# Kernel tuning notes

Hardware: AMD Instinct MI355X
Metric: run time of the kernel (lower is better)

The kernel has to match this reference:

```python
import jax, jax.numpy as jnp
import numpy as np

N = 16384      # nodes
E = 262144     # edges (avg degree 16)
R = 9          # relation types
D_IN = 384     # embed_size
D_H = 768      # hidden_size
N_CLASSES = 5


def setup_inputs() -> dict:
    key = jax.random.key(0)
    ks = jax.random.split(key, 11)
    s = 0.02
    return {
        "x": jax.random.normal(ks[0], (N, D_IN), jnp.float32),
        "edge_index": jax.random.randint(ks[1], (2, E), 0, N, dtype=jnp.int64)
        if jax.config.jax_enable_x64 else jax.random.randint(ks[1], (2, E), 0, N).astype(jnp.int32),
        "edge_type": jax.random.randint(ks[2], (E,), 0, R).astype(jnp.int32),
        "rel_W": jax.random.normal(ks[3], (R, D_H, D_IN), jnp.float32) * s,
        "rel_b": jax.random.normal(ks[4], (R, D_H), jnp.float32) * s,
        "norm_constants": jnp.ones((R,), jnp.float32),
        "mp_lin_W": jax.random.normal(ks[5], (D_H, D_H), jnp.float32) * s,
        "mp_lin_b": jax.random.normal(ks[6], (D_H,), jnp.float32) * s,
        "mp_self_W": jax.random.normal(ks[7], (D_H, D_H), jnp.float32) * s,
        "mp_self_b": jax.random.normal(ks[8], (D_H,), jnp.float32) * s,
        "out_W": jax.random.normal(ks[9], (N_CLASSES, D_H), jnp.float32) * s,
        "out_b": jax.random.normal(ks[10], (N_CLASSES,), jnp.float32) * s,
    }


def reference(x, edge_index, edge_type, rel_W, rel_b, norm_constants,
              mp_lin_W, mp_lin_b, mp_self_W, mp_self_b, out_W, out_b):
    n = x.shape[0]
    src = edge_index[0]  # j : message source (x_j)
    dst = edge_index[1]  # i : aggregation target

    # --- RelationAwareMP ---
    # edge_weights[i, j] from x @ x.T, computed per edge (identical math)
    ew = jnp.einsum('ed,ed->e', x[dst], x[src])                  # [E]
    norm = ew / norm_constants[edge_type]                        # [E]
    # per-relation linear applied to all nodes, then gathered per edge
    h = jnp.einsum('nd,rhd->rnh', x, rel_W) + rel_b[:, None, :]  # [R,N,H]
    msg = h[edge_type, src]                                      # [E,H]
    aggr = jax.ops.segment_sum(norm[:, None] * msg, dst, num_segments=n)
    x1 = jax.nn.relu(aggr)                                       # [N,H]

    # --- MP (add aggregation + self transform) ---
    self_x = x1 @ mp_self_W.T + mp_self_b
    hm = x1 @ mp_lin_W.T + mp_lin_b
    aggr2 = jax.ops.segment_sum(hm[src], dst, num_segments=n)
    x2 = jax.nn.relu(aggr2 + self_x)                             # [N,H]

    # --- readout ---
    pooled = x2.mean(axis=0)                                     # [H]
    return pooled @ out_W.T + out_b                              # [N_CLASSES]
```

## Files before the change

### kernel.cpp

```cpp
#include <hip/hip_runtime.h>

typedef unsigned char  u8;
typedef unsigned short u16;
typedef unsigned int   u32;

#define NN   16384
#define EE   262144
#define RR   9
#define DIN  384
#define DH   768
#define KSU  3456
#define KS   3488
#define NPB  4
#define PCOP 16

typedef float  f32x4 __attribute__((ext_vector_type(4)));
typedef float  f32x2 __attribute__((ext_vector_type(2)));
typedef u32    u32x2 __attribute__((ext_vector_type(2)));
typedef __bf16 b16x8 __attribute__((ext_vector_type(8)));

__device__ __forceinline__ u16 f2bf(float f){
  u32 u = __builtin_bit_cast(u32, f);
  u += 0x7fffu + ((u >> 16) & 1u);
  return (u16)(u >> 16);
}
__device__ __forceinline__ float bf2f(u16 h){
  u32 u = ((u32)h) << 16;
  return __builtin_bit_cast(float, u);
}
__device__ __forceinline__ u32 pkbf(float a, float b){
  return (u32)f2bf(a) | ((u32)f2bf(b) << 16);
}
__device__ __forceinline__ void gll16(const void* g, void* l){
  __builtin_amdgcn_global_load_lds((const __attribute__((address_space(1))) void*)g,
                                   (__attribute__((address_space(3))) void*)l, 16, 0, 0);
}
template<int N> __device__ __forceinline__ float dppror(float v){
  return __builtin_bit_cast(float,
    __builtin_amdgcn_update_dpp(0, __builtin_bit_cast(int, v), 0x120+N, 0xF, 0xF, true));
}
__device__ __forceinline__ float swz16(float v){
  return __builtin_bit_cast(float,
    __builtin_amdgcn_ds_swizzle(__builtin_bit_cast(int, v), 0x401F));
}

__global__ void k_count(const int* __restrict__ dst, int* __restrict__ counts){
  const int e = blockIdx.x*256 + threadIdx.x;
  if (e < EE) atomicAdd(&counts[dst[e]], 1);
}

__global__ __launch_bounds__(1024) void k_scan(const int* __restrict__ counts,
                                               int* __restrict__ starts,
                                               int* __restrict__ cursor){
  __shared__ int tot[1024];
  const int t = threadIdx.x;
  int loc[16]; int s = 0;
  #pragma unroll
  for (int j=0;j<16;j++){ loc[j] = counts[t*16+j]; s += loc[j]; }
  tot[t] = s;
  __syncthreads();
  for (int o=1;o<1024;o<<=1){
    int v = (t>=o) ? tot[t-o] : 0;
    __syncthreads();
    tot[t] += v;
    __syncthreads();
  }
  int run = tot[t] - s;
  #pragma unroll
  for (int j=0;j<16;j++){ starts[t*16+j] = run; cursor[t*16+j] = run; run += loc[j]; }
  if (t == 1023) starts[NN] = run;
}

__global__ void k_place(const int* __restrict__ src, const int* __restrict__ dst,
                        const int* __restrict__ et, int* __restrict__ cursor,
                        int* __restrict__ sp){
  const int e = blockIdx.x*256 + threadIdx.x;
  if (e < EE){
    const int p = atomicAdd(&cursor[dst[e]], 1);
    sp[p] = (int)(((u32)et[e] << 28) | (u32)src[e]);
  }
}

__global__ void k_convW1(const float* __restrict__ rW, const float* __restrict__ rb,
                         u16* __restrict__ Wst){
  const int hh = blockIdx.y;
  const int k  = blockIdx.x*256 + threadIdx.x;
  if (k >= KS) return;
  float v;
  if (k < KSU){ const int r = k / DIN; const int d = k - r*DIN;
                v = rW[((long)r*DH + hh)*DIN + d]; }
  else if (k < KSU + RR){ const int r = k - KSU; v = rb[(long)r*DH + hh]; }
  else v = 0.f;
  Wst[(long)hh*KS + k] = f2bf(v);
}

__global__ void k_convW2(const float* __restrict__ lW, const float* __restrict__ sW,
                         u16* __restrict__ WB){
  const int idx = blockIdx.x*256 + threadIdx.x;
  const float v = (idx < DH*DH) ? lW[idx] : sW[idx - DH*DH];
  WB[idx] = f2bf(v);
}

__global__ __launch_bounds__(256, 3) void k_phase1f(const float* __restrict__ x,
                                                    const int* __restrict__ sp,
                                                    const float* __restrict__ nc,
                                                    const int* __restrict__ starts,
                                                    u16* __restrict__ s){
  const int wv = threadIdx.x >> 6;
  const int l  = threadIdx.x & 63;
  const int i  = blockIdx.x*4 + wv;
  const float* xdp = x + (long)i*DIN;
  const f32x4 xq = *(const f32x4*)(xdp + 4*l);
  const f32x2 xr = *(const f32x2*)(xdp + 256 + 2*l);
  float acc[RR][6];
  float cacc[RR];
  #pragma unroll
  for (int r=0;r<RR;r++){
    cacc[r] = 0.f;
    #pragma unroll
    for (int j=0;j<6;j++) acc[r][j] = 0.f;
  }
  const int e0 = starts[i], e1 = starts[i+1];
  f32x4 Aq={0,0,0,0}, Bq={0,0,0,0}, Cq={0,0,0,0}, Dq={0,0,0,0};
  f32x2 Ar={0,0}, Br={0,0}, Cr={0,0}, Dr={0,0};
  u32 qA=0,qB=0,qC=0,qD=0;
  #define LDE(S, QQ, IDX) { const int pe_=(IDX); if (pe_ < e1){ QQ = (u32)sp[pe_]; \
      const float* xs_ = x + (long)(QQ & 0x3FFFu)*DIN; \
      S##q = *(const f32x4*)(xs_ + 4*l); \
      S##r = *(const f32x2*)(xs_ + 256 + 2*l); } }
  LDE(A,qA,e0) LDE(B,qB,e0+1) LDE(C,qC,e0+2) LDE(D,qD,e0+3)
  #define DOT(uq,ur) (xq.x*uq.x + xq.y*uq.y + xq.z*uq.z + xq.w*uq.w \
                    + xr.x*ur.x + xr.y*ur.y)
  #define UPD(R,P,cq,cr) { cacc[R] += P; \
      acc[R][0] += P*cq.x; acc[R][1] += P*cq.y; acc[R][2] += P*cq.z; \
      acc[R][3] += P*cq.w; acc[R][4] += P*cr.x; acc[R][5] += P*cr.y; }
  #define SW(RQ,P,cq,cr) switch (RQ){ \
      case 0: UPD(0,P,cq,cr); break; case 1: UPD(1,P,cq,cr); break; \
      case 2: UPD(2,P,cq,cr); break; case 3: UPD(3,P,cq,cr); break; \
      case 4: UPD(4,P,cq,cr); break; case 5: UPD(5,P,cq,cr); break; \
      case 6: UPD(6,P,cq,cr); break; case 7: UPD(7,P,cq,cr); break; \
      default: UPD(8,P,cq,cr); break; }
  for (int p=e0; p<e1; p+=4){
    const f32x4 aq=Aq, bq=Bq, cq=Cq, dq=Dq;
    const f32x2 ar=Ar, br=Br, cr=Cr, dr=Dr;
    const u32 qa=qA, qb=qB, qc=qC, qd=qD;
    const bool h1 = p+1<e1, h2 = p+2<e1, h3 = p+3<e1;
    LDE(A,qA,p+4) LDE(B,qB,p+5) LDE(C,qC,p+6) LDE(D,qD,p+7)
    float pa = DOT(aq,ar), pb = DOT(bq,br);
    float pc = DOT(cq,cr), pd = DOT(dq,dr);
    pa += dppror<1>(pa); pb += dppror<1>(pb); pc += dppror<1>(pc); pd += dppror<1>(pd);
    pa += dppror<2>(pa); pb += dppror<2>(pb); pc += dppror<2>(pc); pd += dppror<2>(pd);
    pa += dppror<4>(pa); pb += dppror<4>(pb); pc += dppror<4>(pc); pd += dppror<4>(pd);
    pa += dppror<8>(pa); pb += dppror<8>(pb); pc += dppror<8>(pc); pd += dppror<8>(pd);
    pa += swz16(pa); pb += swz16(pb); pc += swz16(pc); pd += swz16(pd);
    pa += __shfl_xor(pa,32); pb += __shfl_xor(pb,32);
    pc += __shfl_xor(pc,32); pd += __shfl_xor(pd,32);
    SW(qa>>28, pa, aq,ar);
    if (h1){ SW(qb>>28, pb, bq,br); }
    if (h2){ SW(qc>>28, pc, cq,cr); }
    if (h3){ SW(qd>>28, pd, dq,dr); }
  }
  #undef LDE
  #undef DOT
  #undef UPD
  #undef SW
  u16* srow = s + (long)i*KS;
  #pragma unroll
  for (int r=0;r<RR;r++){
    const float inv = 1.0f / nc[r];
    const u32 pk0 = pkbf(acc[r][0]*inv, acc[r][1]*inv);
    const u32 pk1 = pkbf(acc[r][2]*inv, acc[r][3]*inv);
    const u32 pk2 = pkbf(acc[r][4]*inv, acc[r][5]*inv);
    *(u32x2*)(srow + r*DIN + 4*l) = (u32x2){pk0, pk1};
    ((u32*)(srow + r*DIN + 256))[l] = pk2;
  }
  float cv = 0.f;
  #pragma unroll
  for (int r=0;r<RR;r++) cv = (l == r) ? cacc[r] : cv;
  if (l < 32){
    const float invl = (l < RR) ? 1.0f/nc[l] : 0.f;
    srow[KSU + l] = f2bf(l < RR ? cv*invl : 0.f);
  }
}

template<int MODE, int NT>
__global__ __launch_bounds__(256, 3)
void k_gemm128r(const u16* __restrict__ A, const u16* __restrict__ B, int K,
                u16* __restrict__ O0, u16* __restrict__ O1,
                const float* __restrict__ b0, const float* __restrict__ b1)
{
  __shared__ __align__(16) u16 lds[3][2][128*32];
  const int cpx = gridDim.x >> 3;
  const int bid = blockIdx.x;
  const int lg  = (bid & 7)*cpx + (bid >> 3);
  const int mt  = lg / NT;
  const long m0 = (long)mt * 128;
  const long n0 = (long)(lg - mt*NT) * 128;
  const int t   = threadIdx.x;
  const int wv  = t >> 6;
  const int ln  = t & 63;
  const int wm  = wv >> 1, wn = wv & 1;
  const int fr  = ln & 15, fq = ln >> 4;

  const int arow = t >> 2;
  const int gsl  = (t & 3) ^ ((arow >> 1) & 3);

  f32x4 acc[4][4];
  #pragma unroll
  for (int i=0;i<4;i++)
    #pragma unroll
    for (int j=0;j<4;j++) acc[i][j] = {0.f,0.f,0.f,0.f};

  const int nk = K >> 5;

  #define STAGE(SL, TT) { const long k0_ = (long)(TT)*32;                         \
    u16* sa_ = &lds[SL][0][0]; u16* sb_ = &lds[SL][1][0];                         \
    gll16(A + (m0 +      arow)*(long)K + k0_ + gsl*8, sa_ + wv*512);              \
    gll16(A + (m0 + 64 + arow)*(long)K + k0_ + gsl*8, sa_ + 2048 + wv*512);       \
    gll16(B + (n0 +      arow)*(long)K + k0_ + gsl*8, sb_ + wv*512);              \
    gll16(B + (n0 + 64 + arow)*(long)K + k0_ + gsl*8, sb_ + 2048 + wv*512); }

  STAGE(0, 0) STAGE(1, 1)
  asm volatile("s_waitcnt vmcnt(4)" ::: "memory");
  __builtin_amdgcn_s_barrier();

  int cs = 0, ps = 2;
  for (int tt = 0; tt < nk; ++tt){
    if (tt + 2 < nk) STAGE(ps, tt + 2)
    const u16* sa = &lds[cs][0][0];
    const u16* sb = &lds[cs][1][0];
    b16x8 av[4], bv[4];
    #pragma unroll
    for (int i=0;i<4;i++){
      const int row = wm*64 + i*16 + fr;
      av[i] = *(const b16x8*)((const u8*)sa + row*64 + ((fq ^ ((row>>1)&3)) << 4));
    }
    #pragma unroll
    for (int j=0;j<4;j++){
      const int row = wn*64 + j*16 + fr;
      bv[j] = *(const b16x8*)((const u8*)sb + row*64 + ((fq ^ ((row>>1)&3)) << 4));
    }
    __builtin_amdgcn_s_setprio(1);
    #pragma unroll
    for (int i=0;i<4;i++)
      #pragma unroll
      for (int j=0;j<4;j++)
        acc[i][j] = __builtin_amdgcn_mfma_f32_16x16x32_bf16(av[i], bv[j], acc[i][j], 0, 0, 0);
    __builtin_amdgcn_s_setprio(0);
    if (tt + 2 < nk)      asm volatile("s_waitcnt vmcnt(4)" ::: "memory");
    else if (tt + 1 < nk) asm volatile("s_waitcnt vmcnt(0)" ::: "memory");
    __builtin_amdgcn_s_barrier();
    cs = (cs == 2) ? 0 : cs + 1;
    ps = (ps == 2) ? 0 : ps + 1;
  }
  #undef STAGE

  #pragma unroll
  for (int i=0;i<4;i++){
    #pragma unroll
    for (int j=0;j<4;j++){
      #pragma unroll
      for (int r=0;r<4;r++){
        const long m = m0 + wm*64 + i*16 + fq*4 + r;
        const long n = n0 + wn*64 + j*16 + fr;
        float v = acc[i][j][r];
        if (MODE == 0){
          v = v > 0.f ? v : 0.f;
          O0[m*DH + n] = f2bf(v);
        } else {
          if (n < DH) O0[m*DH + n]      = f2bf(v + b0[n]);
          else        O1[m*DH + (n-DH)] = f2bf(v + b1[n-DH]);
        }
      }
    }
  }
}

__global__ __launch_bounds__(128) void k_phase2(const u16* __restrict__ hm,
                                                const u16* __restrict__ sfx,
                                                const int* __restrict__ sp,
                                                const int* __restrict__ starts,
                                                float* __restrict__ pooledP){
  const int t  = threadIdx.x;
  const int i0 = blockIdx.x * NPB;
  const int p0 = starts[i0];
  const int pend = starts[i0 + NPB];
  u32 sf00,sf01,sf02, sf10,sf11,sf12, sf20,sf21,sf22, sf30,sf31,sf32;
  { const u32* sr = (const u32*)(sfx + (long)(i0+0)*DH); sf00=sr[t]; sf01=sr[t+128]; sf02=sr[t+256]; }
  { const u32* sr = (const u32*)(sfx + (long)(i0+1)*DH); sf10=sr[t]; sf11=sr[t+128]; sf12=sr[t+256]; }
  { const u32* sr = (const u32*)(sfx + (long)(i0+2)*DH); sf20=sr[t]; sf21=sr[t+128]; sf22=sr[t+256]; }
  { const u32* sr = (const u32*)(sfx + (long)(i0+3)*DH); sf30=sr[t]; sf31=sr[t+128]; sf32=sr[t+256]; }
  u32 A0=0,A1=0,A2=0,B0=0,B1=0,B2=0,C0=0,C1=0,C2=0,D0=0,D1=0,D2=0;
  u32 E0=0,E1=0,E2=0,F0=0,F1=0,F2=0,G0=0,G1=0,G2=0,H0=0,H1=0,H2=0;
  #define PLD(S, IDX) { const int nf_=(IDX); if (nf_ < pend){ \
      const u32* hr_ = (const u32*)(hm + (long)(((u32)sp[nf_]) & 0x3FFFu)*DH); \
      S##0=hr_[t]; S##1=hr_[t+128]; S##2=hr_[t+256]; } }
  PLD(A,p0)   PLD(B,p0+1) PLD(C,p0+2) PLD(D,p0+3)
  PLD(E,p0+4) PLD(F,p0+5) PLD(G,p0+6) PLD(H,p0+7)
  float a0=0.f,a1=0.f,a2=0.f,a3=0.f,a4=0.f,a5=0.f;
  float q0=0.f,q1=0.f,q2=0.f,q3=0.f,q4=0.f,q5=0.f;
  int i = i0;
  int e1 = starts[i0+1];
  #define FLUSH(K) { float v_; \
    v_=a0+bf2f((u16)sf##K##0);        q0+=fmaxf(v_,0.f); \
    v_=a1+bf2f((u16)(sf##K##0>>16));  q1+=fmaxf(v_,0.f); \
    v_=a2+bf2f((u16)sf##K##1);        q2+=fmaxf(v_,0.f); \
    v_=a3+bf2f((u16)(sf##K##1>>16));  q3+=fmaxf(v_,0.f); \
    v_=a4+bf2f((u16)sf##K##2);        q4+=fmaxf(v_,0.f); \
    v_=a5+bf2f((u16)(sf##K##2>>16));  q5+=fmaxf(v_,0.f); \
    a0=a1=a2=a3=a4=a5=0.f; }
  #define FLUSHI { switch (i - i0){ case 0: FLUSH(0); break; case 1: FLUSH(1); break; \
                   case 2: FLUSH(2); break; default: FLUSH(3); break; } }
  while (i < i0+NPB && e1 == p0){ FLUSHI; ++i; e1 = (i < i0+NPB) ? starts[i+1] : 0x7fffffff; }
  #define STEP(S, K) { const int pe_ = base + K; if (pe_ < pend){ \
      const u32 d0_=S##0, d1_=S##1, d2_=S##2; \
      PLD(S, pe_ + 8); \
      a0+=bf2f((u16)d0_); a1+=bf2f((u16)(d0_>>16)); \
      a2+=bf2f((u16)d1_); a3+=bf2f((u16)(d1_>>16)); \
      a4+=bf2f((u16)d2_); a5+=bf2f((u16)(d2_>>16)); \
      while (i < i0+NPB && pe_+1 == e1){ FLUSHI; ++i; \
        e1 = (i < i0+NPB) ? starts[i+1] : 0x7fffffff; } } }
  for (int base = p0; base < pend; base += 8){
    STEP(A,0) STEP(B,1) STEP(C,2) STEP(D,3)
    STEP(E,4) STEP(F,5) STEP(G,6) STEP(H,7)
  }
  while (i < i0+NPB){ FLUSHI; ++i; }
  #undef PLD
  #undef FLUSH
  #undef FLUSHI
  #undef STEP
  float* pd = pooledP + (blockIdx.x & (PCOP-1)) * DH;
  atomicAdd(&pd[2*t],       q0);
  atomicAdd(&pd[2*t+1],     q1);
  atomicAdd(&pd[256+2*t],   q2);
  atomicAdd(&pd[256+2*t+1], q3);
  atomicAdd(&pd[512+2*t],   q4);
  atomicAdd(&pd[512+2*t+1], q5);
}

__global__ __launch_bounds__(256) void k_final(const float* __restrict__ pooledP,
                                               const float* __restrict__ oW,
                                               const float* __restrict__ ob,
                                               float* __restrict__ out){
  __shared__ float ps[DH];
  __shared__ float red[256];
  const int t = threadIdx.x;
  for (int h=t; h<DH; h+=256){
    float s = 0.f;
    #pragma unroll
    for (int c=0;c<PCOP;c++) s += pooledP[c*DH + h];
    ps[h] = s;
  }
  __syncthreads();
  for (int c=0;c<5;c++){
    float p = 0.f;
    for (int h=t; h<DH; h+=256) p += ps[h]*oW[c*DH + h];
    red[t] = p; __syncthreads();
    for (int o=128;o;o>>=1){ if (t<o) red[t]+=red[t+o]; __syncthreads(); }
    if (t == 0) out[c] = red[0]*(1.f/(float)NN) + ob[c];
    __syncthreads();
  }
}

extern "C" void kernel_launch(void* const* d_in, const int* in_sizes, int n_in,
                              void* d_out, int out_size, void* d_ws, size_t ws_size,
                              hipStream_t stream)
{
  (void)in_sizes; (void)n_in; (void)out_size; (void)ws_size;
  const float* x     = (const float*)d_in[0];
  const int*   ei    = (const int*)  d_in[1];
  const int*   et    = (const int*)  d_in[2];
  const float* relW  = (const float*)d_in[3];
  const float* relb  = (const float*)d_in[4];
  const float* nc    = (const float*)d_in[5];
  const float* linW  = (const float*)d_in[6];
  const float* linb  = (const float*)d_in[7];
  const float* selfW = (const float*)d_in[8];
  const float* selfb = (const float*)d_in[9];
  const float* outW  = (const float*)d_in[10];
  const float* outb  = (const float*)d_in[11];
  float* out = (float*)d_out;

  u8* w = (u8*)d_ws;
  int*   counts = (int*)(w + 0);
  int*   starts = (int*)(w + 65536);
  int*   cursor = (int*)(w + 131328);
  int*   srcp   = (int*)(w + 196864);
  u16*   Wst    = (u16*)(w + 4391168);
  u16*   WB     = (u16*)(w + 9748736);
  u16*   x1     = (u16*)(w + 12108032);
  u16*   S      = (u16*)(w + 37276928);
  u16*   hm     = S;
  u16*   sfx    = (u16*)(w + 37276928 + 25165824);
  float* pooledP = (float*)(w + 37276928 + 50331648);

  const int* esrc = ei;
  const int* edst = ei + EE;

  hipMemsetAsync(counts, 0, NN*sizeof(int), stream);

  k_count <<<EE/256, 256, 0, stream>>>(edst, counts);
  k_scan  <<<1, 1024, 0, stream>>>(counts, starts, cursor);
  k_place <<<EE/256, 256, 0, stream>>>(esrc, edst, et, cursor, srcp);
  k_convW1<<<dim3(14, DH), 256, 0, stream>>>(relW, relb, Wst);
  k_convW2<<<(2*DH*DH)/256, 256, 0, stream>>>(linW, selfW, WB);
  k_phase1f<<<NN/4, 256, 0, stream>>>(x, srcp, nc, starts, S);
  k_gemm128r<0,6><<<(NN/128)*(DH/128), 256, 0, stream>>>(
      S, Wst, KS, x1, (u16*)nullptr, (const float*)nullptr, (const float*)nullptr);
  hipMemsetAsync(pooledP, 0, PCOP*DH*sizeof(float), stream);
  k_gemm128r<1,12><<<(NN/128)*(2*DH/128), 256, 0, stream>>>(
      x1, WB, DH, hm, sfx, linb, selfb);
  k_phase2<<<NN/NPB, 128, 0, stream>>>(hm, sfx, srcp, starts, pooledP);
  k_final <<<1, 256, 0, stream>>>(pooledP, outW, outb, out);
}
```

Baseline: 461.4 us.

## Widen GEMM tiles to 256x128 with 512 threads; halve phase2 nodes per block

Both bf16 GEMMs now use 256x128 output tiles computed by 8 waves, where each block previously computed a 128x128 tile with 4 waves. Each B tile staged in LDS is shared by twice as many rows, which cuts global and LDS staging traffic per output element. LDS fragment addresses are precomputed once, since the XOR swizzle only depends on the lane. Separately, the phase2 gather kernel now handles 2 nodes per block instead of 4, giving more blocks and fewer live registers per thread. The trade-off is that larger GEMM blocks halve the block count and use more LDS per block, which can reduce occupancy and worsen load balance across CUs.

After: 463.3 us. About the same (+0.4%).

```diff
diff --git a/kernel.cpp b/kernel.cpp
--- a/kernel.cpp
+++ b/kernel.cpp
@@ -11,7 +11,7 @@
 #define DH   768
 #define KSU  3456
 #define KS   3488
-#define NPB  4
+#define NPB  2
 #define PCOP 16
 
 typedef float  f32x4 __attribute__((ext_vector_type(4)));
@@ -184,27 +184,32 @@
 }
 
 template<int MODE, int NT>
-__global__ __launch_bounds__(256, 3)
-void k_gemm128r(const u16* __restrict__ A, const u16* __restrict__ B, int K,
-                u16* __restrict__ O0, u16* __restrict__ O1,
-                const float* __restrict__ b0, const float* __restrict__ b1)
+__global__ __launch_bounds__(512, 4)
+void k_gemmw(const u16* __restrict__ A, const u16* __restrict__ B, int K,
+             u16* __restrict__ O0, u16* __restrict__ O1,
+             const float* __restrict__ b0, const float* __restrict__ b1)
 {
-  __shared__ __align__(16) u16 lds[3][2][128*32];
+  __shared__ __align__(16) u16 lds[3][(256+128)*32];
   const int cpx = gridDim.x >> 3;
   const int bid = blockIdx.x;
   const int lg  = (bid & 7)*cpx + (bid >> 3);
   const int mt  = lg / NT;
-  const long m0 = (long)mt * 128;
+  const long m0 = (long)mt * 256;
   const long n0 = (long)(lg - mt*NT) * 128;
   const int t   = threadIdx.x;
   const int wv  = t >> 6;
   const int ln  = t & 63;
-  const int wm  = wv >> 1, wn = wv & 1;
+  const int wm  = wv >> 1;
+  const int wn  = wv & 1;
   const int fr  = ln & 15, fq = ln >> 4;
 
   const int arow = t >> 2;
   const int gsl  = (t & 3) ^ ((arow >> 1) & 3);
 
+  const int su    = fq ^ ((fr >> 1) & 3);
+  const int dsA   = (wm*64 + fr)*64 + (su << 4);
+  const int dsB   = 16384 + (wn*64 + fr)*64 + (su << 4);
+
   f32x4 acc[4][4];
   #pragma unroll
   for (int i=0;i<4;i++)
@@ -214,32 +219,24 @@
   const int nk = K >> 5;
 
   #define STAGE(SL, TT) { const long k0_ = (long)(TT)*32;                         \
-    u16* sa_ = &lds[SL][0][0]; u16* sb_ = &lds[SL][1][0];                         \
-    gll16(A + (m0 +      arow)*(long)K + k0_ + gsl*8, sa_ + wv*512);              \
-    gll16(A + (m0 + 64 + arow)*(long)K + k0_ + gsl*8, sa_ + 2048 + wv*512);       \
-    gll16(B + (n0 +      arow)*(long)K + k0_ + gsl*8, sb_ + wv*512);              \
-    gll16(B + (n0 + 64 + arow)*(long)K + k0_ + gsl*8, sb_ + 2048 + wv*512); }
+    u16* s_ = &lds[SL][0];                                                        \
+    gll16(A + (m0 +       arow)*(long)K + k0_ + gsl*8, s_ + wv*512);              \
+    gll16(A + (m0 + 128 + arow)*(long)K + k0_ + gsl*8, s_ + 4096 + wv*512);       \
+    gll16(B + (n0 +       arow)*(long)K + k0_ + gsl*8, s_ + 8192 + wv*512); }
 
   STAGE(0, 0) STAGE(1, 1)
-  asm volatile("s_waitcnt vmcnt(4)" ::: "memory");
+  asm volatile("s_waitcnt vmcnt(3)" ::: "memory");
   __builtin_amdgcn_s_barrier();
 
   int cs = 0, ps = 2;
   for (int tt = 0; tt < nk; ++tt){
     if (tt + 2 < nk) STAGE(ps, tt + 2)
-    const u16* sa = &lds[cs][0][0];
-    const u16* sb = &lds[cs][1][0];
+    const u8* sl = (const u8*)&lds[cs][0];
     b16x8 av[4], bv[4];
     #pragma unroll
-    for (int i=0;i<4;i++){
-      const int row = wm*64 + i*16 + fr;
-      av[i] = *(const b16x8*)((const u8*)sa + row*64 + ((fq ^ ((row>>1)&3)) << 4));
-    }
-    #pragma unroll
-    for (int j=0;j<4;j++){
-      const int row = wn*64 + j*16 + fr;
-      bv[j] = *(const b16x8*)((const u8*)sb + row*64 + ((fq ^ ((row>>1)&3)) << 4));
-    }
+    for (int i=0;i<4;i++) av[i] = *(const b16x8*)(sl + dsA + i*1024);
+    #pragma unroll
+    for (int j=0;j<4;j++) bv[j] = *(const b16x8*)(sl + dsB + j*1024);
     __builtin_amdgcn_s_setprio(1);
     #pragma unroll
     for (int i=0;i<4;i++)
@@ -247,7 +244,7 @@
       for (int j=0;j<4;j++)
         acc[i][j] = __builtin_amdgcn_mfma_f32_16x16x32_bf16(av[i], bv[j], acc[i][j], 0, 0, 0);
     __builtin_amdgcn_s_setprio(0);
-    if (tt + 2 < nk)      asm volatile("s_waitcnt vmcnt(4)" ::: "memory");
+    if (tt + 2 < nk)      asm volatile("s_waitcnt vmcnt(3)" ::: "memory");
     else if (tt + 1 < nk) asm volatile("s_waitcnt vmcnt(0)" ::: "memory");
     __builtin_amdgcn_s_barrier();
     cs = (cs == 2) ? 0 : cs + 1;
@@ -285,11 +282,9 @@
   const int i0 = blockIdx.x * NPB;
   const int p0 = starts[i0];
   const int pend = starts[i0 + NPB];
-  u32 sf00,sf01,sf02, sf10,sf11,sf12, sf20,sf21,sf22, sf30,sf31,sf32;
+  u32 sf00,sf01,sf02, sf10,sf11,sf12;
   { const u32* sr = (const u32*)(sfx + (long)(i0+0)*DH); sf00=sr[t]; sf01=sr[t+128]; sf02=sr[t+256]; }
   { const u32* sr = (const u32*)(sfx + (long)(i0+1)*DH); sf10=sr[t]; sf11=sr[t+128]; sf12=sr[t+256]; }
-  { const u32* sr = (const u32*)(sfx + (long)(i0+2)*DH); sf20=sr[t]; sf21=sr[t+128]; sf22=sr[t+256]; }
-  { const u32* sr = (const u32*)(sfx + (long)(i0+3)*DH); sf30=sr[t]; sf31=sr[t+128]; sf32=sr[t+256]; }
   u32 A0=0,A1=0,A2=0,B0=0,B1=0,B2=0,C0=0,C1=0,C2=0,D0=0,D1=0,D2=0;
   u32 E0=0,E1=0,E2=0,F0=0,F1=0,F2=0,G0=0,G1=0,G2=0,H0=0,H1=0,H2=0;
   #define PLD(S, IDX) { const int nf_=(IDX); if (nf_ < pend){ \
@@ -309,8 +304,7 @@
     v_=a4+bf2f((u16)sf##K##2);        q4+=fmaxf(v_,0.f); \
     v_=a5+bf2f((u16)(sf##K##2>>16));  q5+=fmaxf(v_,0.f); \
     a0=a1=a2=a3=a4=a5=0.f; }
-  #define FLUSHI { switch (i - i0){ case 0: FLUSH(0); break; case 1: FLUSH(1); break; \
-                   case 2: FLUSH(2); break; default: FLUSH(3); break; } }
+  #define FLUSHI { if (i == i0){ FLUSH(0); } else { FLUSH(1); } }
   while (i < i0+NPB && e1 == p0){ FLUSHI; ++i; e1 = (i < i0+NPB) ? starts[i+1] : 0x7fffffff; }
   #define STEP(S, K) { const int pe_ = base + K; if (pe_ < pend){ \
       const u32 d0_=S##0, d1_=S##1, d2_=S##2; \
@@ -405,10 +399,10 @@
   k_convW1<<<dim3(14, DH), 256, 0, stream>>>(relW, relb, Wst);
   k_convW2<<<(2*DH*DH)/256, 256, 0, stream>>>(linW, selfW, WB);
   k_phase1f<<<NN/4, 256, 0, stream>>>(x, srcp, nc, starts, S);
-  k_gemm128r<0,6><<<(NN/128)*(DH/128), 256, 0, stream>>>(
+  k_gemmw<0,6><<<(NN/256)*(DH/128), 512, 0, stream>>>(
       S, Wst, KS, x1, (u16*)nullptr, (const float*)nullptr, (const float*)nullptr);
   hipMemsetAsync(pooledP, 0, PCOP*DH*sizeof(float), stream);
-  k_gemm128r<1,12><<<(NN/128)*(2*DH/128), 256, 0, stream>>>(
+  k_gemmw<1,12><<<(NN/256)*(2*DH/128), 512, 0, stream>>>(
       x1, WB, DH, hm, sfx, linb, selfb);
   k_phase2<<<NN/NPB, 128, 0, stream>>>(hm, sfx, srcp, starts, pooledP);
   k_final <<<1, 256, 0, stream>>>(pooledP, outW, outb, out);
```
